# Kernel tuning notes

Measured on AMD Instinct MI355X. Metric: run time of the kernel, lower is better.

Reference implementation:

```python
import jax, jax.numpy as jnp
import numpy as np

B, S, D_IN, D_H = 8, 4096, 256, 512
EPS = 1e-6


def setup_inputs() -> dict:
    key = jax.random.key(0)
    ks = jax.random.split(key, 5)
    scale = 1.0 / np.sqrt(D_IN)  # torch Linear default init scale (uniform bound)
    x = jax.random.normal(ks[0], (B, S, D_IN), dtype=jnp.float32)
    Wi = jax.random.normal(ks[1], (D_IN, D_H), dtype=jnp.float32) * scale
    Wf = jax.random.normal(ks[2], (D_IN, D_H), dtype=jnp.float32) * scale
    Wo = jax.random.normal(ks[3], (D_IN, D_H), dtype=jnp.float32) * scale
    Wz = jax.random.normal(ks[4], (D_IN, D_H), dtype=jnp.float32) * scale
    zb = jnp.zeros((D_H,), dtype=jnp.float32)
    return {"x": x, "Wi": Wi, "bi": zb, "Wf": Wf, "bf": zb,
            "Wo": Wo, "bo": zb, "Wz": Wz, "bz": zb}


def _xlstm_forward(x, Wi, bi, Wf, bf, Wo, bo, Wz, bz):
    # Batched projections over all timesteps at once: [B,S,D_H] each.
    i_t = jnp.exp(jnp.clip(jnp.einsum('bsd,dh->bsh', x, Wi) + bi, -20.0, 0.0))
    f_t = jnp.exp(jnp.clip(jnp.einsum('bsd,dh->bsh', x, Wf) + bf, -20.0, 0.0))
    o_t = jax.nn.sigmoid(jnp.einsum('bsd,dh->bsh', x, Wo) + bo)
    z_t = jnp.tanh(jnp.einsum('bsd,dh->bsh', x, Wz) + bz)

    def step(carry, gates):
        c, n = carry
        i, f, o, z = gates
        c = f * c + i * z
        n = f * n + i
        h = o * (c / (n + EPS))
        return (c, n), h

    c0 = jnp.zeros((x.shape[0], Wi.shape[1]), dtype=x.dtype)
    n0 = jnp.ones((x.shape[0], Wi.shape[1]), dtype=x.dtype)
    # time-major scan over the recurrence
    gates_tm = tuple(jnp.swapaxes(g, 0, 1) for g in (i_t, f_t, o_t, z_t))  # [S,B,H]
    _, h_tm = jax.lax.scan(step, (c0, n0), gates_tm)
    return jnp.swapaxes(h_tm, 0, 1)  # [B,S,H]


def reference(x, Wi, bi, Wf, bf, Wo, bo, Wz, bz):
    return _xlstm_forward(x, Wi, bi, Wf, bf, Wo, bo, Wz, bz)
```

## Files before the change

kernel.cpp:

```cpp
#include <hip/hip_runtime.h>
#include <hip/hip_bf16.h>
#include <cstdint>
#include <cstddef>

typedef __hip_bfloat16 bf16;
typedef __attribute__((ext_vector_type(8))) short short8;
typedef __attribute__((ext_vector_type(4))) short short4v;
typedef __attribute__((ext_vector_type(4))) float floatx4;

#define BB 8
#define SS 4096
#define DIN 256
#define DH 512
#define NCH 128
#define CHUNK 32

__device__ __forceinline__ float b2f(bf16 v) { return __bfloat162float(v); }
__device__ __forceinline__ float sh2f(short v) {
    unsigned int u = ((unsigned int)(unsigned short)v) << 16;
    float f; __builtin_memcpy(&f, &u, 4); return f;
}
__device__ __forceinline__ float frcp(float x) { return __builtin_amdgcn_rcpf(x); }
__device__ __forceinline__ short f2sh(float a) {
    bf16 bv = __float2bfloat16(a);
    short sv; __builtin_memcpy(&sv, &bv, 2); return sv;
}

__global__ __launch_bounds__(256) void convert_x(
    const float* __restrict__ X, bf16* __restrict__ Xb)
{
    const int idx = blockIdx.x * 256 + threadIdx.x;
    float4 v = ((const float4*)X)[idx];
    bf16 o[4] = {__float2bfloat16(v.x), __float2bfloat16(v.y),
                 __float2bfloat16(v.z), __float2bfloat16(v.w)};
    ((short4v*)Xb)[idx] = *(const short4v*)o;
}

__global__ __launch_bounds__(256) void transpose_w(
    const float* __restrict__ Wi, const float* __restrict__ Wf,
    const float* __restrict__ Wo, const float* __restrict__ Wz,
    bf16* __restrict__ Wt)
{
    int o = blockIdx.x * 256 + threadIdx.x;
    int r = o >> 8;
    int k = o & 255;
    int y = r >> 7;
    int c = r & 127;
    int g = c >> 5;
    int h = y * 32 + (c & 31);
    const float* W = (g == 0) ? Wi : (g == 1) ? Wf : (g == 2) ? Wo : Wz;
    Wt[o] = __float2bfloat16(W[(size_t)k * DH + h]);
}

__device__ __forceinline__ void load16_lds(const bf16* g, short* l)
{
    __builtin_amdgcn_global_load_lds(
        (const __attribute__((address_space(1))) unsigned int*)g,
        (__attribute__((address_space(3))) unsigned int*)l,
        16, 0, 0);
}

__global__ __launch_bounds__(256) void gemm_mfma(
    const bf16* __restrict__ Xb, const bf16* __restrict__ Wt,
    const float* __restrict__ bi, const float* __restrict__ bfv,
    const float* __restrict__ bo, const float* __restrict__ bz,
    bf16* __restrict__ Pi, bf16* __restrict__ Pf,
    bf16* __restrict__ Po, bf16* __restrict__ Pz,
    float* __restrict__ Aa, float* __restrict__ Bca, float* __restrict__ Bna,
    int nb)
{
    __shared__ __align__(16) short smem[128 * 132];
    short* As = smem;
    short* Bs = smem + 4096;

    const int tid  = threadIdx.x;
    const int m0   = blockIdx.x * 128;
    const int y    = blockIdx.y;
    const int n0   = y * 128;
    const int wave = tid >> 6, lane = tid & 63;
    const int wm   = (wave >> 1) * 64, wn = (wave & 1) * 64;
    const int l15  = lane & 15;
    const int q    = lane >> 4;

    floatx4 acc[4][4];
#pragma unroll
    for (int i = 0; i < 4; i++)
#pragma unroll
        for (int j = 0; j < 4; j++) acc[i][j] = (floatx4){0.f, 0.f, 0.f, 0.f};

    const int r_ld = tid >> 2;
    const int c_ld = tid & 3;
    const bf16* agp0 = Xb + (size_t)(m0 + r_ld) * DIN + c_ld * 8;
    const bf16* agp1 = Xb + (size_t)(m0 + 64 + r_ld) * DIN + c_ld * 8;
    const bf16* bgp0 = Wt + (size_t)(n0 + r_ld) * DIN + c_ld * 8;
    const bf16* bgp1 = Wt + (size_t)(n0 + 64 + r_ld) * DIN + c_ld * 8;

    for (int k0 = 0; k0 < DIN; k0 += 32) {
        load16_lds(agp0 + k0, &As[tid * 8]);
        load16_lds(agp1 + k0, &As[2048 + tid * 8]);
        load16_lds(bgp0 + k0, &Bs[tid * 8]);
        load16_lds(bgp1 + k0, &Bs[2048 + tid * 8]);
        __syncthreads();

        short8 af[4], bfr[4];
#pragma unroll
        for (int ti = 0; ti < 4; ti++)
            af[ti] = *(const short8*)&As[(wm + ti * 16 + l15) * 32 + q * 8];
#pragma unroll
        for (int tj = 0; tj < 4; tj++)
            bfr[tj] = *(const short8*)&Bs[(wn + tj * 16 + l15) * 32 + q * 8];
#pragma unroll
        for (int ti = 0; ti < 4; ti++)
#pragma unroll
            for (int tj = 0; tj < 4; tj++)
                acc[ti][tj] = __builtin_amdgcn_mfma_f32_16x16x32_bf16(
                    af[ti], bfr[tj], acc[ti][tj], 0, 0, 0);
        __syncthreads();
    }

#pragma unroll
    for (int ti = 0; ti < 4; ti++) {
        const int mrow = wm + ti * 16 + q * 4;
#pragma unroll
        for (int tj = 0; tj < 4; tj++) {
            const int cb = wn + tj * 16;
            const int g  = cb >> 5;
            const int c  = cb + l15;
            const float* bp = (g == 0) ? bi : (g == 1) ? bfv
                            : (g == 2) ? bo : bz;
            const float bsv = bp[y * 32 + (c & 31)];
#pragma unroll
            for (int r = 0; r < 4; r++) {
                const float v = acc[ti][tj][r] + bsv;
                float a;
                if (g == 0 || g == 1) {
                    a = __expf(fminf(fmaxf(v, -20.f), 0.f));
                } else if (g == 2) {
                    a = frcp(1.f + __expf(-v));
                } else {
                    a = 1.f - 2.f * frcp(__expf(2.f * v) + 1.f);
                }
                smem[(mrow + r) * 132 + c] = f2sh(a);
            }
        }
    }
    __syncthreads();

    const int bidx = m0 / SS;

    {
        const int cp  = (tid & 31) * 4;
        const int g2  = cp >> 5;
        const int hb  = y * 32 + (cp & 31);
        bf16* pl = ((g2 == 0) ? Pi : (g2 == 1) ? Pf : (g2 == 2) ? Po : Pz) + hb;
        const int r0 = tid >> 5;
#pragma unroll
        for (int t = 0; t < 16; t++) {
            const int row = t * 8 + r0;
            short4v v = *(const short4v*)&smem[row * 132 + cp];
            *(short4v*)(pl + (size_t)(m0 + row) * DH) = v;
        }
    }

    if (tid < 128) {
        const int hh = tid & 31;
        const int ch = tid >> 5;
        float A = 1.f, Bc = 0.f, Bn = 0.f;
        const short* base = &smem[(ch * 32) * 132];
#pragma unroll 8
        for (int s = 0; s < CHUNK; s++) {
            const short* rp = base + s * 132;
            const float iv = sh2f(rp[hh]);
            const float f  = sh2f(rp[32 + hh]);
            const float zv = sh2f(rp[96 + hh]);
            Bc = fmaf(f, Bc, iv * zv);
            Bn = fmaf(f, Bn, iv);
            A *= f;
        }
        const int ch_g = ((m0 % SS) >> 5) + ch;
        const int hgl  = y * 32 + hh;
        const size_t cidx = (size_t)(ch_g * nb + bidx) * DH + hgl;
        Aa[cidx] = A; Bca[cidx] = Bc; Bna[cidx] = Bn;
    }
}

__global__ __launch_bounds__(256) void scan_chunks(
    const float* __restrict__ Aa, const float* __restrict__ Bca,
    const float* __restrict__ Bna,
    float* __restrict__ Cs, float* __restrict__ Ns, int nb)
{
    const int t = blockIdx.x * 256 + threadIdx.x;
    float c = 0.f, n = 1.f;
    for (int ch = 0; ch < NCH; ch++) {
        const size_t cidx = (size_t)ch * (nb * DH) + t;
        Cs[cidx] = c; Ns[cidx] = n;
        const float A = Aa[cidx];
        c = fmaf(A, c, Bca[cidx]);
        n = fmaf(A, n, Bna[cidx]);
    }
}

__global__ __launch_bounds__(256) void scan_emit(
    const bf16* __restrict__ Pi, const bf16* __restrict__ Pf,
    const bf16* __restrict__ Po, const bf16* __restrict__ Pz,
    const float* __restrict__ Cs, const float* __restrict__ Ns,
    float* __restrict__ out, int nb)
{
    const int tid = threadIdx.x;
    const int ch  = blockIdx.x * 4 + (tid >> 6);
    const int b   = blockIdx.y;
    const int hg  = (tid & 63) * 8;
    const size_t base = ((size_t)(b * SS + ch * CHUNK)) * DH + hg;
    const size_t cidx = (size_t)(ch * nb + b) * DH + hg;

    float c[8], n[8];
#pragma unroll
    for (int j = 0; j < 2; j++) {
        *(floatx4*)&c[j * 4] = *(const floatx4*)(Cs + cidx + j * 4);
        *(floatx4*)&n[j * 4] = *(const floatx4*)(Ns + cidx + j * 4);
    }

#pragma unroll 4
    for (int s = 0; s < CHUNK; s++) {
        const size_t o = base + (size_t)s * DH;
        short8 i8 = *(const short8*)(Pi + o);
        short8 f8 = *(const short8*)(Pf + o);
        short8 o8 = *(const short8*)(Po + o);
        short8 z8 = *(const short8*)(Pz + o);
        float h[8];
#pragma unroll
        for (int j = 0; j < 8; j++) {
            const float f  = sh2f(f8[j]);
            const float iv = sh2f(i8[j]);
            const float ov = sh2f(o8[j]);
            const float zv = sh2f(z8[j]);
            c[j] = fmaf(f, c[j], iv * zv);
            n[j] = fmaf(f, n[j], iv);
            h[j] = ov * c[j] * frcp(n[j] + 1e-6f);
        }
        *(floatx4*)(out + o)     = *(floatx4*)&h[0];
        *(floatx4*)(out + o + 4) = *(floatx4*)&h[4];
    }
}

extern "C" void kernel_launch(void* const* d_in, const int* in_sizes, int n_in,
                              void* d_out, int out_size, void* d_ws, size_t ws_size,
                              hipStream_t stream)
{
    const float* x   = (const float*)d_in[0];
    const float* Wi  = (const float*)d_in[1];
    const float* bi  = (const float*)d_in[2];
    const float* Wf  = (const float*)d_in[3];
    const float* bfv = (const float*)d_in[4];
    const float* Wo  = (const float*)d_in[5];
    const float* bo  = (const float*)d_in[6];
    const float* Wz  = (const float*)d_in[7];
    const float* bz  = (const float*)d_in[8];
    float* out = (float*)d_out;

    int nb = BB;
    while (nb > 1) {
        size_t need = (1u << 20)
                    + (size_t)nb * SS * DIN * 2
                    + 4 * (size_t)nb * SS * DH * 2
                    + 5 * (size_t)NCH * nb * DH * 4;
        if (need <= ws_size) break;
        nb >>= 1;
    }

    const size_t plane = (size_t)nb * SS * DH;
    bf16* Wt = (bf16*)d_ws;
    bf16* Xb = (bf16*)((char*)d_ws + (1u << 20));
    bf16* Pi = Xb + (size_t)nb * SS * DIN;
    bf16* Pf = Pi + plane;
    bf16* Po = Pf + plane;
    bf16* Pz = Po + plane;
    float* Aa  = (float*)(Pz + plane);
    float* Bca = Aa  + (size_t)NCH * nb * DH;
    float* Bna = Bca + (size_t)NCH * nb * DH;
    float* Cs  = Bna + (size_t)NCH * nb * DH;
    float* Ns  = Cs  + (size_t)NCH * nb * DH;

    transpose_w<<<2048, 256, 0, stream>>>(Wi, Wf, Wo, Wz, Wt);

    for (int b0 = 0; b0 < BB; b0 += nb) {
        const float* Xsrc = x   + (size_t)b0 * SS * DIN;
        float*       Ob   = out + (size_t)b0 * SS * DH;
        convert_x<<<nb * 1024, 256, 0, stream>>>(Xsrc, Xb);
        gemm_mfma<<<dim3(nb * SS / 128, 16), 256, 0, stream>>>(
            Xb, Wt, bi, bfv, bo, bz, Pi, Pf, Po, Pz, Aa, Bca, Bna, nb);
        scan_chunks<<<2 * nb, 256, 0, stream>>>(Aa, Bca, Bna, Cs, Ns, nb);
        scan_emit<<<dim3(NCH / 4, nb), 256, 0, stream>>>(
            Pi, Pf, Po, Pz, Cs, Ns, Ob, nb);
    }
}
```

Measured before the change: 237.6 us.

## Double-buffer GEMM LDS loads, halve scan chunk size, reuse chunk buffers in place

```diff
diff --git a/kernel.cpp b/kernel.cpp
--- a/kernel.cpp
+++ b/kernel.cpp
@@ -12,8 +12,8 @@
 #define SS 4096
 #define DIN 256
 #define DH 512
-#define NCH 128
-#define CHUNK 32
+#define NCH 256
+#define CHUNK 16
 
 __device__ __forceinline__ float b2f(bf16 v) { return __bfloat162float(v); }
 __device__ __forceinline__ float sh2f(short v) {
@@ -70,12 +70,10 @@
     int nb)
 {
     __shared__ __align__(16) short smem[128 * 132];
-    short* As = smem;
-    short* Bs = smem + 4096;
 
     const int tid  = threadIdx.x;
-    const int m0   = blockIdx.x * 128;
-    const int y    = blockIdx.y;
+    const int y    = blockIdx.x;
+    const int m0   = blockIdx.y * 128;
     const int n0   = y * 128;
     const int wave = tid >> 6, lane = tid & 63;
     const int wm   = (wave >> 1) * 64, wn = (wave & 1) * 64;
@@ -95,28 +93,43 @@
     const bf16* bgp0 = Wt + (size_t)(n0 + r_ld) * DIN + c_ld * 8;
     const bf16* bgp1 = Wt + (size_t)(n0 + 64 + r_ld) * DIN + c_ld * 8;
 
-    for (int k0 = 0; k0 < DIN; k0 += 32) {
-        load16_lds(agp0 + k0, &As[tid * 8]);
-        load16_lds(agp1 + k0, &As[2048 + tid * 8]);
-        load16_lds(bgp0 + k0, &Bs[tid * 8]);
-        load16_lds(bgp1 + k0, &Bs[2048 + tid * 8]);
-        __syncthreads();
-
+#define STAGE(K0, BUF)                                            \
+    do {                                                          \
+        short* A_ = smem + (BUF) * 8192;                          \
+        short* B_ = A_ + 4096;                                    \
+        load16_lds(agp0 + (K0), &A_[tid * 8]);                    \
+        load16_lds(agp1 + (K0), &A_[2048 + tid * 8]);             \
+        load16_lds(bgp0 + (K0), &B_[tid * 8]);                    \
+        load16_lds(bgp1 + (K0), &B_[2048 + tid * 8]);             \
+    } while (0)
+
+    STAGE(0, 0);
+    asm volatile("s_waitcnt vmcnt(0)" ::: "memory");
+    __builtin_amdgcn_s_barrier();
+
+#pragma unroll
+    for (int k = 0; k < 8; k++) {
+        const int cur = k & 1;
+        if (k < 7) STAGE((k + 1) * 32, cur ^ 1);
+        const short* A = smem + cur * 8192;
+        const short* B = A + 4096;
         short8 af[4], bfr[4];
 #pragma unroll
         for (int ti = 0; ti < 4; ti++)
-            af[ti] = *(const short8*)&As[(wm + ti * 16 + l15) * 32 + q * 8];
+            af[ti] = *(const short8*)&A[(wm + ti * 16 + l15) * 32 + q * 8];
 #pragma unroll
         for (int tj = 0; tj < 4; tj++)
-            bfr[tj] = *(const short8*)&Bs[(wn + tj * 16 + l15) * 32 + q * 8];
+            bfr[tj] = *(const short8*)&B[(wn + tj * 16 + l15) * 32 + q * 8];
 #pragma unroll
         for (int ti = 0; ti < 4; ti++)
 #pragma unroll
             for (int tj = 0; tj < 4; tj++)
                 acc[ti][tj] = __builtin_amdgcn_mfma_f32_16x16x32_bf16(
                     af[ti], bfr[tj], acc[ti][tj], 0, 0, 0);
-        __syncthreads();
-    }
+        asm volatile("s_waitcnt vmcnt(0) lgkmcnt(0)" ::: "memory");
+        __builtin_amdgcn_s_barrier();
+    }
+#undef STAGE
 
 #pragma unroll
     for (int ti = 0; ti < 4; ti++) {
@@ -162,12 +175,12 @@
         }
     }
 
-    if (tid < 128) {
+    {
         const int hh = tid & 31;
         const int ch = tid >> 5;
         float A = 1.f, Bc = 0.f, Bn = 0.f;
-        const short* base = &smem[(ch * 32) * 132];
-#pragma unroll 8
+        const short* base = &smem[(ch * CHUNK) * 132];
+#pragma unroll
         for (int s = 0; s < CHUNK; s++) {
             const short* rp = base + s * 132;
             const float iv = sh2f(rp[hh]);
@@ -177,7 +190,7 @@
             Bn = fmaf(f, Bn, iv);
             A *= f;
         }
-        const int ch_g = ((m0 % SS) >> 5) + ch;
+        const int ch_g = ((m0 % SS) >> 4) + ch;
         const int hgl  = y * 32 + hh;
         const size_t cidx = (size_t)(ch_g * nb + bidx) * DH + hgl;
         Aa[cidx] = A; Bca[cidx] = Bc; Bna[cidx] = Bn;
@@ -185,18 +198,19 @@
 }
 
 __global__ __launch_bounds__(256) void scan_chunks(
-    const float* __restrict__ Aa, const float* __restrict__ Bca,
-    const float* __restrict__ Bna,
-    float* __restrict__ Cs, float* __restrict__ Ns, int nb)
+    float* __restrict__ Aa, float* __restrict__ Bca,
+    const float* __restrict__ Bna, int nb)
 {
     const int t = blockIdx.x * 256 + threadIdx.x;
     float c = 0.f, n = 1.f;
     for (int ch = 0; ch < NCH; ch++) {
         const size_t cidx = (size_t)ch * (nb * DH) + t;
-        Cs[cidx] = c; Ns[cidx] = n;
-        const float A = Aa[cidx];
-        c = fmaf(A, c, Bca[cidx]);
-        n = fmaf(A, n, Bna[cidx]);
+        const float A  = Aa[cidx];
+        const float Bc = Bca[cidx];
+        const float Bn = Bna[cidx];
+        Aa[cidx] = c; Bca[cidx] = n;
+        c = fmaf(A, c, Bc);
+        n = fmaf(A, n, Bn);
     }
 }
 
@@ -263,7 +277,7 @@
         size_t need = (1u << 20)
                     + (size_t)nb * SS * DIN * 2
                     + 4 * (size_t)nb * SS * DH * 2
-                    + 5 * (size_t)NCH * nb * DH * 4;
+                    + 3 * (size_t)NCH * nb * DH * 4;
         if (need <= ws_size) break;
         nb >>= 1;
     }
@@ -278,8 +292,6 @@
     float* Aa  = (float*)(Pz + plane);
     float* Bca = Aa  + (size_t)NCH * nb * DH;
     float* Bna = Bca + (size_t)NCH * nb * DH;
-    float* Cs  = Bna + (size_t)NCH * nb * DH;
-    float* Ns  = Cs  + (size_t)NCH * nb * DH;
 
     transpose_w<<<2048, 256, 0, stream>>>(Wi, Wf, Wo, Wz, Wt);
 
@@ -287,10 +299,10 @@
         const float* Xsrc = x   + (size_t)b0 * SS * DIN;
         float*       Ob   = out + (size_t)b0 * SS * DH;
         convert_x<<<nb * 1024, 256, 0, stream>>>(Xsrc, Xb);
-        gemm_mfma<<<dim3(nb * SS / 128, 16), 256, 0, stream>>>(
+        gemm_mfma<<<dim3(16, nb * SS / 128), 256, 0, stream>>>(
             Xb, Wt, bi, bfv, bo, bz, Pi, Pf, Po, Pz, Aa, Bca, Bna, nb);
-        scan_chunks<<<2 * nb, 256, 0, stream>>>(Aa, Bca, Bna, Cs, Ns, nb);
+        scan_chunks<<<2 * nb, 256, 0, stream>>>(Aa, Bca, Bna, nb);
         scan_emit<<<dim3(NCH / 4, nb), 256, 0, stream>>>(
-            Pi, Pf, Po, Pz, Cs, Ns, Ob, nb);
-    }
-}
+            Pi, Pf, Po, Pz, Aa, Bca, Ob, nb);
+    }
+}
```

Result: slower. 253.9 us (+6.9%).
